# Kernel tuning notes

Hardware: AMD Instinct MI355X
Metric: run time of the kernel (lower is better)

## Reference

```python
import jax, jax.numpy as jnp
import numpy as np

N_HEADS = 16


def apply_rotary_emb(x, cos, sin):
    # x: [B, H, S, hd]; cos/sin: [S, hd//2] (broadcast over B, H)
    xr = x.reshape(x.shape[:-1] + (-1, 2))
    r, i = xr[..., 0], xr[..., 1]
    a = r * cos - i * sin
    b = i * cos + r * sin
    return jnp.stack([a, b], axis=-1).reshape(x.shape).astype(x.dtype)


def setup_inputs() -> dict:
    key = jax.random.key(0)
    ks = jax.random.split(key, 7)
    B, S, D = 2, 2048, 1024
    hd = D // N_HEADS
    x = jax.random.normal(ks[0], (B, S, D), dtype=jnp.float32)
    freqs_cos = jax.random.uniform(ks[1], (S, hd // 2), dtype=jnp.float32)
    freqs_sin = jax.random.uniform(ks[2], (S, hd // 2), dtype=jnp.float32)
    sc = 1.0 / np.sqrt(D)
    Wq = jax.random.normal(ks[3], (D, D), dtype=jnp.float32) * sc
    Wk = jax.random.normal(ks[4], (D, D), dtype=jnp.float32) * sc
    Wv = jax.random.normal(ks[5], (D, D), dtype=jnp.float32) * sc
    Wo = jax.random.normal(ks[6], (D, D), dtype=jnp.float32) * sc
    return {"x": x, "freqs_cos": freqs_cos, "freqs_sin": freqs_sin,
            "Wq": Wq, "Wk": Wk, "Wv": Wv, "Wo": Wo}


def reference(x, freqs_cos, freqs_sin, Wq, Wk, Wv, Wo):
    B, S, D = x.shape
    H = N_HEADS
    hd = D // H
    # QKV projections (nn.Linear: x @ W.T)
    q = (x @ Wq.T).reshape(B, S, H, hd).transpose(0, 2, 1, 3)
    k = (x @ Wk.T).reshape(B, S, H, hd).transpose(0, 2, 1, 3)
    v = (x @ Wv.T).reshape(B, S, H, hd).transpose(0, 2, 1, 3)
    q = apply_rotary_emb(q, freqs_cos, freqs_sin)
    k = apply_rotary_emb(k, freqs_cos, freqs_sin)
    # causal SDPA (scale = 1/sqrt(head_dim), as in F.scaled_dot_product_attention)
    scores = jnp.einsum("bhqd,bhkd->bhqk", q, k) * (1.0 / np.sqrt(hd))
    causal = jnp.tril(jnp.ones((S, S), dtype=bool))
    scores = jnp.where(causal, scores, -jnp.inf)
    probs = jax.nn.softmax(scores, axis=-1)
    attn_out = jnp.einsum("bhqk,bhkd->bhqd", probs, v)
    attn_cat = attn_out.transpose(0, 2, 1, 3).reshape(B, S, D)
    return attn_cat @ Wo.T
```

## Files before the change

### kernel.cpp

```cpp
#include <hip/hip_runtime.h>
#include <hip/hip_bf16.h>
#include <cstdint>

typedef __attribute__((ext_vector_type(8))) short short8;
typedef __attribute__((ext_vector_type(4))) float f32x4;

#define B_  2
#define S_  2048
#define D_  1024
#define H_  16
#define HD  64

static __device__ __forceinline__ float bf2f(unsigned int u16) {
    union { unsigned int i; float f; } v; v.i = u16 << 16; return v.f;
}
static __device__ __forceinline__ unsigned short f2bf(float f) {
    union { float f; unsigned int i; } v; v.f = f;
    unsigned int r = v.i + 0x7FFFu + ((v.i >> 16) & 1u);
    return (unsigned short)(r >> 16);
}
static __device__ __forceinline__ unsigned pack_bf16(float hi, float lo) {
    union { float f; unsigned u; } h, l;
    h.f = hi; l.f = lo;
    return __builtin_amdgcn_perm(h.u + 0x8000u, l.u + 0x8000u, 0x07060302);
}
static __device__ __forceinline__ unsigned cvt_pk_bf16(float a, float b) {
    unsigned r;
    asm("v_cvt_pk_bf16_f32 %0, %1, %2" : "=v"(r) : "v"(a), "v"(b));
    return r;
}
static __device__ __forceinline__ void load_lds_16B(const unsigned short* g, unsigned short* l) {
    __builtin_amdgcn_global_load_lds(
        (const __attribute__((address_space(1))) unsigned int*)g,
        (__attribute__((address_space(3))) unsigned int*)l, 16, 0, 0);
}

__global__ void cvt_all(const float* __restrict__ x,
                        const float* __restrict__ w0, const float* __restrict__ w1,
                        const float* __restrict__ w2, const float* __restrict__ w3,
                        unsigned short* __restrict__ xbf,
                        unsigned short* __restrict__ wdst) {
    int bid = blockIdx.x;
    if (bid < 4096) {
        int i = bid * 256 + threadIdx.x;
        float4 f = ((const float4*)x)[i];
        uint2 o;
        o.x = (unsigned int)f2bf(f.x) | ((unsigned int)f2bf(f.y) << 16);
        o.y = (unsigned int)f2bf(f.z) | ((unsigned int)f2bf(f.w) << 16);
        ((uint2*)xbf)[i] = o;
    } else {
        int wb = bid - 4096;
        int wsel = wb >> 10;
        const float* s = wsel == 0 ? w0 : wsel == 1 ? w1 : wsel == 2 ? w2 : w3;
        int i = (wb & 1023) * 256 + threadIdx.x;
        float4 f = ((const float4*)s)[i];
        uint2 o;
        o.x = (unsigned int)f2bf(f.x) | ((unsigned int)f2bf(f.y) << 16);
        o.y = (unsigned int)f2bf(f.z) | ((unsigned int)f2bf(f.w) << 16);
        ((uint2*)wdst)[(size_t)wsel * 262144 + i] = o;
    }
}

__global__ __launch_bounds__(256) void qkv_gemm(
    const unsigned short* __restrict__ xbf,
    const unsigned short* __restrict__ wq,
    const unsigned short* __restrict__ wk,
    const unsigned short* __restrict__ wv,
    const float* __restrict__ fcos,
    const float* __restrict__ fsin,
    unsigned short* __restrict__ qb,
    unsigned short* __restrict__ kb,
    unsigned short* __restrict__ vb)
{
    __shared__ unsigned short pool[2][2][128 * 32];

    const int tid  = threadIdx.x;
    const int w    = tid >> 6, lane = tid & 63;
    const int l15  = lane & 15, quad = lane >> 4;
    const int wrow = (w >> 1) * 64, wcol = (w & 1) * 64;

    const int m0 = blockIdx.x * 128;
    const int nc = blockIdx.y * 128;
    const int sel = nc >> 10;
    const int n0 = nc & 1023;
    const unsigned short* __restrict__ W = sel == 0 ? wq : (sel == 1 ? wk : wv);

    const int lr = lane >> 2, lc = (lane & 3) * 8;
    const unsigned short* ga = xbf + (size_t)(m0 + w * 16 + lr) * 1024 + lc;
    const unsigned short* gb = W   + (size_t)(n0 + w * 16 + lr) * 1024 + lc;

    f32x4 acc[4][4] = {};

    auto STAGE = [&](int k0, int bufi) {
        load_lds_16B(ga + k0,             &pool[bufi][0][(w * 16) * 32]);
        load_lds_16B(ga + 64 * 1024 + k0, &pool[bufi][0][(64 + w * 16) * 32]);
        load_lds_16B(gb + k0,             &pool[bufi][1][(w * 16) * 32]);
        load_lds_16B(gb + 64 * 1024 + k0, &pool[bufi][1][(64 + w * 16) * 32]);
    };

    STAGE(0, 0);
    __syncthreads();

    int cur = 0;
    for (int k0 = 0; k0 < 1024; k0 += 32) {
        if (k0 + 32 < 1024) STAGE(k0 + 32, cur ^ 1);

        short8 a[4], b[4];
#pragma unroll
        for (int i = 0; i < 4; i++)
            a[i] = *(const short8*)&pool[cur][0][(wrow + i * 16 + l15) * 32 + quad * 8];
#pragma unroll
        for (int j = 0; j < 4; j++)
            b[j] = *(const short8*)&pool[cur][1][(wcol + j * 16 + l15) * 32 + quad * 8];
#pragma unroll
        for (int i = 0; i < 4; i++)
#pragma unroll
            for (int j = 0; j < 4; j++)
                acc[i][j] = __builtin_amdgcn_mfma_f32_16x16x32_bf16(a[i], b[j], acc[i][j], 0, 0, 0);

        __syncthreads();
        cur ^= 1;
    }

    if (sel == 2) {
        unsigned short (*Tt)[136] = reinterpret_cast<unsigned short (*)[136]>(&pool[0][0][0]);
        const int bb  = blockIdx.x >> 4;
        const int m0s = (blockIdx.x & 15) * 128;
        const int h0  = n0 >> 6;
        const int nh  = w & 1;
#pragma unroll
        for (int half = 0; half < 2; half++) {
            __syncthreads();
            if (nh == half) {
#pragma unroll
                for (int i = 0; i < 4; i++)
#pragma unroll
                    for (int j = 0; j < 4; j++) {
                        uint2 pk;
                        pk.x = pack_bf16(acc[i][j][1], acc[i][j][0]);
                        pk.y = pack_bf16(acc[i][j][3], acc[i][j][2]);
                        *(uint2*)&Tt[j * 16 + l15][wrow + i * 16 + quad * 4] = pk;
                    }
            }
            __syncthreads();
            const int row = tid >> 2, cq = tid & 3;
            unsigned short* vrow = vb +
                (((size_t)(bb * H_ + h0 + half)) * HD + row) * S_ + m0s + cq * 32;
#pragma unroll
            for (int k = 0; k < 4; k++) {
                short8 v = *(const short8*)&Tt[row][cq * 32 + k * 8];
                *(short8*)(vrow + k * 8) = v;
            }
        }
    } else {
        unsigned short* __restrict__ Out = sel == 0 ? qb : kb;
        const float qsc = (sel == 0) ? 0.125f * 1.44269504f : 1.0f;
        const int odd = l15 & 1;
#pragma unroll
        for (int i = 0; i < 4; i++)
#pragma unroll
            for (int r = 0; r < 4; r++) {
                int m = m0 + wrow + i * 16 + quad * 4 + r;
                int bb = m >> 11, s = m & 2047;
#pragma unroll
                for (int j = 0; j < 4; j++) {
                    int n = n0 + wcol + j * 16 + l15;
                    int h = n >> 6, d = n & 63;
                    int t = d >> 1;
                    float c  = fcos[s * 32 + t];
                    float si = fsin[s * 32 + t];
                    float own = acc[i][j][r];
                    float oth = __shfl_xor(own, 1, 64);
                    float outv = odd ? (own * c + oth * si) : (own * c - oth * si);
                    Out[(((size_t)(bb * H_ + h) * S_) + s) * HD + d] = f2bf(outv * qsc);
                }
            }
    }
}

__global__ __launch_bounds__(256) void out_gemm(
    const unsigned short* __restrict__ A,
    const unsigned short* __restrict__ Bt,
    float* __restrict__ C)
{
    __shared__ __attribute__((aligned(1024))) unsigned short Apool[2][128 * 64];
    __shared__ __attribute__((aligned(1024))) unsigned short Bpool[2][64 * 64];

    const int tid  = threadIdx.x;
    const int w    = tid >> 6, lane = tid & 63;
    const int l15  = lane & 15, quad = lane >> 4;
    const int wrow = (w >> 1) * 64, wcol = (w & 1) * 32;

    const int m0 = blockIdx.x * 128;
    const int n0 = blockIdx.y * 64;

    const int srow  = lane >> 3;
    const int sslot = (lane & 7) ^ srow;
    const int s7    = l15 & 7;

    f32x4 acc[4][2] = {};

    auto STAGE = [&](int k0, int bufi) {
        const unsigned short* gaa = A + (size_t)m0 * 1024 + k0 + sslot * 8;
        load_lds_16B(gaa + (size_t)(w * 16 + srow) * 1024,          &Apool[bufi][(w * 16) * 64]);
        load_lds_16B(gaa + (size_t)(w * 16 + 8 + srow) * 1024,      &Apool[bufi][(w * 16 + 8) * 64]);
        load_lds_16B(gaa + (size_t)(64 + w * 16 + srow) * 1024,     &Apool[bufi][(64 + w * 16) * 64]);
        load_lds_16B(gaa + (size_t)(64 + w * 16 + 8 + srow) * 1024, &Apool[bufi][(64 + w * 16 + 8) * 64]);
        const unsigned short* gbb = Bt + (size_t)n0 * 1024 + k0 + sslot * 8;
        load_lds_16B(gbb + (size_t)(w * 16 + srow) * 1024,          &Bpool[bufi][(w * 16) * 64]);
        load_lds_16B(gbb + (size_t)(w * 16 + 8 + srow) * 1024,      &Bpool[bufi][(w * 16 + 8) * 64]);
    };

    STAGE(0, 0);
    __syncthreads();

    int cur = 0;
    for (int k0 = 0; k0 < 1024; k0 += 64) {
        if (k0 + 64 < 1024) STAGE(k0 + 64, cur ^ 1);

        short8 a[4][2], b[2][2];
#pragma unroll
        for (int kk = 0; kk < 2; kk++) {
#pragma unroll
            for (int i = 0; i < 4; i++) {
                int row = wrow + i * 16 + l15;
                int slot = (((kk << 2) | quad) ^ s7) << 4;
                a[i][kk] = *(const short8*)((const char*)&Apool[cur][0] + (row << 7) + slot);
            }
#pragma unroll
            for (int j = 0; j < 2; j++) {
                int row = wcol + j * 16 + l15;
                int slot = (((kk << 2) | quad) ^ s7) << 4;
                b[j][kk] = *(const short8*)((const char*)&Bpool[cur][0] + (row << 7) + slot);
            }
        }
#pragma unroll
        for (int kk = 0; kk < 2; kk++)
#pragma unroll
            for (int i = 0; i < 4; i++)
#pragma unroll
                for (int j = 0; j < 2; j++)
                    acc[i][j] = __builtin_amdgcn_mfma_f32_16x16x32_bf16(a[i][kk], b[j][kk], acc[i][j], 0, 0, 0);

        __syncthreads();
        cur ^= 1;
    }

#pragma unroll
    for (int i = 0; i < 4; i++)
#pragma unroll
        for (int r = 0; r < 4; r++) {
            int m = m0 + wrow + i * 16 + quad * 4 + r;
#pragma unroll
            for (int j = 0; j < 2; j++)
                C[(size_t)m * 1024 + n0 + wcol + j * 16 + l15] = acc[i][j][r];
        }
}

__global__ __launch_bounds__(256) void flash_attn_mfma(
    const unsigned short* __restrict__ qb,
    const unsigned short* __restrict__ kb,
    const unsigned short* __restrict__ vT,
    unsigned short* __restrict__ attnc)
{
    __shared__ __attribute__((aligned(1024))) unsigned short Ks[2][2][64][32];
    __shared__ __attribute__((aligned(1024))) unsigned short Vt[64][64];
    __shared__ unsigned short Pls[4][16][72];

    const int bh   = blockIdx.x;
    const int qtb  = blockIdx.y;
    const int jj = qtb & 7, mm = qtb >> 3;
    const int qt = (mm == 0) ? jj : (mm == 1) ? 31 - jj : (mm == 2) ? 8 + jj : 23 - jj;

    const int b    = bh >> 4, h = bh & 15;
    const int tid  = threadIdx.x;
    const int w    = tid >> 6;
    const int lane = tid & 63;
    const int l15  = lane & 15;
    const int quad = lane >> 4;

    const size_t bhS = (size_t)bh * S_;
    const unsigned short* __restrict__ vTb = vT + (size_t)bh * HD * S_;

    short8 qfrag[2];
    {
        const unsigned short* qp = qb + (bhS + qt * 64 + w * 16 + l15) * HD + quad * 8;
        qfrag[0] = *(const short8*)(qp);
        qfrag[1] = *(const short8*)(qp + 32);
    }

    const int ksrow  = lane >> 2;
    const int ksslot = (lane & 3) ^ ((lane >> 3) & 3);
    const int vsrow  = lane >> 3;
    const int vsslot = (lane & 7) ^ vsrow;

    const int ckq = (quad ^ ((l15 >> 1) & 3)) << 4;
    const int s7  = l15 & 7;

    short8 ones;
#pragma unroll
    for (int i = 0; i < 8; i++) ones[i] = (short)0x3F80;

    f32x4 O[4] = {};
    f32x4 Osum = {};
    float mrow = -INFINITY;

    auto STAGE_K = [&](int jt, int bufi) {
        const int j0 = jt * 64;
        const unsigned short* kg = kb + (bhS + j0 + w * 16 + ksrow) * HD + ksslot * 8;
        load_lds_16B(kg,      &Ks[bufi][0][w * 16][0]);
        load_lds_16B(kg + 32, &Ks[bufi][1][w * 16][0]);
    };
    auto STAGE_V = [&](int jt) {
        const int j0 = jt * 64;
        const unsigned short* vg = vTb + (size_t)(w * 16 + vsrow) * S_ + j0 + vsslot * 8;
        load_lds_16B(vg,          &Vt[w * 16][0]);
        load_lds_16B(vg + 8 * S_, &Vt[w * 16 + 8][0]);
    };

    STAGE_K(0, 0);

    for (int jt = 0; jt <= qt; jt++) {
        const int cur = jt & 1;
        asm volatile("s_waitcnt vmcnt(0)" ::: "memory");
        __builtin_amdgcn_s_barrier();

        STAGE_V(jt);
        if (jt < qt) STAGE_K(jt + 1, cur ^ 1);

        const bool diag  = (jt == qt);
        const int  nsub  = diag ? (w + 1) : 4;
        const int  kgmax = (nsub + 1) >> 1;

        f32x4 Sacc[4];
        float tmax = -INFINITY;
        for (int sub = 0; sub < nsub; sub++) {
            f32x4 s = {};
#pragma unroll
            for (int kh = 0; kh < 2; kh++) {
                int bo = ((sub * 16 + l15) << 6) + ckq;
                short8 kf = *(const short8*)((const char*)&Ks[cur][kh][0][0] + bo);
                s = __builtin_amdgcn_mfma_f32_16x16x32_bf16(kf, qfrag[kh], s, 0, 0, 0);
            }
            if (diag) {
#pragma unroll
                for (int r = 0; r < 4; r++)
                    if (sub * 16 + quad * 4 + r > w * 16 + l15) s[r] = -INFINITY;
            }
            float sm = fmaxf(fmaxf(s[0], s[1]), fmaxf(s[2], s[3]));
            tmax = fmaxf(tmax, sm);
            Sacc[sub] = s;
        }
        tmax = fmaxf(tmax, __shfl_xor(tmax, 16, 64));
        tmax = fmaxf(tmax, __shfl_xor(tmax, 32, 64));

        if (__any(tmax > mrow + 8.0f)) {
            float mnew = fmaxf(mrow, tmax);
            float ccr  = __builtin_amdgcn_exp2f(mrow - mnew);
#pragma unroll
            for (int r = 0; r < 4; r++) {
                float ccq = __shfl(ccr, quad * 4 + r, 64);
#pragma unroll
                for (int dt = 0; dt < 4; dt++) O[dt][r] *= ccq;
                Osum[r] *= ccq;
            }
            mrow = mnew;
        }

        for (int sub = 0; sub < nsub; sub++) {
            f32x4 s = Sacc[sub];
            float p0 = __builtin_amdgcn_exp2f(s[0] - mrow);
            float p1 = __builtin_amdgcn_exp2f(s[1] - mrow);
            float p2 = __builtin_amdgcn_exp2f(s[2] - mrow);
            float p3 = __builtin_amdgcn_exp2f(s[3] - mrow);
            uint2 pk;
            pk.x = cvt_pk_bf16(p0, p1);
            pk.y = cvt_pk_bf16(p2, p3);
            *(uint2*)&Pls[w][l15][sub * 16 + quad * 4] = pk;
        }
        if (diag) {
            for (int sub = nsub; sub < 2 * kgmax; sub++) {
                uint2 z; z.x = 0u; z.y = 0u;
                *(uint2*)&Pls[w][l15][sub * 16 + quad * 4] = z;
            }
        }

        if (jt < qt) {
            asm volatile("s_waitcnt vmcnt(2)" ::: "memory");
        } else {
            asm volatile("s_waitcnt vmcnt(0)" ::: "memory");
        }
        __builtin_amdgcn_s_barrier();

        for (int kg = 0; kg < kgmax; kg++) {
            short8 pf = *(const short8*)&Pls[w][l15][kg * 32 + quad * 8];
#pragma unroll
            for (int dt = 0; dt < 4; dt++) {
                int row = dt * 16 + l15;
                int slot = (((kg << 2) | quad) ^ s7) << 4;
                short8 vf = *(const short8*)((const char*)&Vt[0][0] + (row << 7) + slot);
                O[dt] = __builtin_amdgcn_mfma_f32_16x16x32_bf16(pf, vf, O[dt], 0, 0, 0);
            }
            Osum = __builtin_amdgcn_mfma_f32_16x16x32_bf16(pf, ones, Osum, 0, 0, 0);
        }
    }

#pragma unroll
    for (int r = 0; r < 4; r++) {
        float invq = 1.0f / Osum[r];
        int qabs = qt * 64 + w * 16 + quad * 4 + r;
        unsigned short* op = attnc + (((size_t)b * S_ + qabs) * H_ + h) * HD + l15;
#pragma unroll
        for (int dt = 0; dt < 4; dt++)
            op[dt * 16] = f2bf(O[dt][r] * invq);
    }
}

extern "C" void kernel_launch(void* const* d_in, const int* in_sizes, int n_in,
                              void* d_out, int out_size, void* d_ws, size_t ws_size,
                              hipStream_t stream) {
    const float* x    = (const float*)d_in[0];
    const float* fcos = (const float*)d_in[1];
    const float* fsin = (const float*)d_in[2];
    const float* Wq   = (const float*)d_in[3];
    const float* Wk   = (const float*)d_in[4];
    const float* Wv   = (const float*)d_in[5];
    const float* Wo   = (const float*)d_in[6];
    float* out = (float*)d_out;

    unsigned short* ws = (unsigned short*)d_ws;
    unsigned short* xbf = ws;
    unsigned short* wqb = xbf + 4096 * 1024;
    unsigned short* wkb = wqb + 1024 * 1024;
    unsigned short* wvb = wkb + 1024 * 1024;
    unsigned short* wob = wvb + 1024 * 1024;
    unsigned short* qb  = wob + 1024 * 1024;
    unsigned short* kb  = qb + 4096 * 1024;
    unsigned short* vb  = kb + 4096 * 1024;
    unsigned short* attnc = vb + 4096 * 1024;

    cvt_all<<<8192, 256, 0, stream>>>(x, Wq, Wk, Wv, Wo, xbf, wqb);

    qkv_gemm<<<dim3(32, 24), 256, 0, stream>>>(xbf, wqb, wkb, wvb, fcos, fsin, qb, kb, vb);

    flash_attn_mfma<<<dim3(32, 32), 256, 0, stream>>>(qb, kb, vb, attnc);

    out_gemm<<<dim3(32, 16), 256, 0, stream>>>(attnc, wob, out);
}
```

Baseline: 201.7 us.

## Pair causal query tiles per block to share K/V loads and balance work

Each attention block now handles two query tiles, qt and 31-qt, so every block does the same amount of causal work. The K/V tiles staged into LDS are reused by both query tiles, which halves global K/V traffic per query. The grid shrinks from 1024 to 512 blocks. In exchange, register pressure roughly doubles (two sets of O accumulators and Q fragments) and the P scratch buffer doubles, which may reduce occupancy.

```diff
diff --git a/kernel.cpp b/kernel.cpp
--- a/kernel.cpp
+++ b/kernel.cpp
@@ -265,12 +265,12 @@
 {
     __shared__ __attribute__((aligned(1024))) unsigned short Ks[2][2][64][32];
     __shared__ __attribute__((aligned(1024))) unsigned short Vt[64][64];
-    __shared__ unsigned short Pls[4][16][72];
-
-    const int bh   = blockIdx.x;
-    const int qtb  = blockIdx.y;
-    const int jj = qtb & 7, mm = qtb >> 3;
-    const int qt = (mm == 0) ? jj : (mm == 1) ? 31 - jj : (mm == 2) ? 8 + jj : 23 - jj;
+    __shared__ unsigned short Pls[2][4][16][72];
+
+    const int bh    = blockIdx.x;
+    const int qtA   = blockIdx.y;
+    const int qtB   = 31 - qtA;
+    const int jtmax = qtB;
 
     const int b    = bh >> 4, h = bh & 15;
     const int tid  = threadIdx.x;
@@ -282,11 +282,14 @@
     const size_t bhS = (size_t)bh * S_;
     const unsigned short* __restrict__ vTb = vT + (size_t)bh * HD * S_;
 
-    short8 qfrag[2];
+    short8 qfA[2], qfB[2];
     {
-        const unsigned short* qp = qb + (bhS + qt * 64 + w * 16 + l15) * HD + quad * 8;
-        qfrag[0] = *(const short8*)(qp);
-        qfrag[1] = *(const short8*)(qp + 32);
+        const unsigned short* qp = qb + (bhS + qtA * 64 + w * 16 + l15) * HD + quad * 8;
+        qfA[0] = *(const short8*)(qp);
+        qfA[1] = *(const short8*)(qp + 32);
+        const unsigned short* qp2 = qb + (bhS + qtB * 64 + w * 16 + l15) * HD + quad * 8;
+        qfB[0] = *(const short8*)(qp2);
+        qfB[1] = *(const short8*)(qp2 + 32);
     }
 
     const int ksrow  = lane >> 2;
@@ -301,9 +304,11 @@
 #pragma unroll
     for (int i = 0; i < 8; i++) ones[i] = (short)0x3F80;
 
-    f32x4 O[4] = {};
-    f32x4 Osum = {};
-    float mrow = -INFINITY;
+    f32x4 OA[4] = {}, OB[4] = {};
+    f32x4 OsA = {}, OsB = {};
+    float mA = -INFINITY, mB = -INFINITY;
+
+    int cur = 0;
 
     auto STAGE_K = [&](int jt, int bufi) {
         const int j0 = jt * 64;
@@ -318,20 +323,10 @@
         load_lds_16B(vg + 8 * S_, &Vt[w * 16 + 8][0]);
     };
 
-    STAGE_K(0, 0);
-
-    for (int jt = 0; jt <= qt; jt++) {
-        const int cur = jt & 1;
-        asm volatile("s_waitcnt vmcnt(0)" ::: "memory");
-        __builtin_amdgcn_s_barrier();
-
-        STAGE_V(jt);
-        if (jt < qt) STAGE_K(jt + 1, cur ^ 1);
-
-        const bool diag  = (jt == qt);
-        const int  nsub  = diag ? (w + 1) : 4;
-        const int  kgmax = (nsub + 1) >> 1;
-
+    auto QKSM = [&](const short8* qf, float& mrow, f32x4* O, f32x4& Osum,
+                    int psel, bool diag) -> int {
+        const int nsub  = diag ? (w + 1) : 4;
+        const int kgmax = (nsub + 1) >> 1;
         f32x4 Sacc[4];
         float tmax = -INFINITY;
         for (int sub = 0; sub < nsub; sub++) {
@@ -340,7 +335,7 @@
             for (int kh = 0; kh < 2; kh++) {
                 int bo = ((sub * 16 + l15) << 6) + ckq;
                 short8 kf = *(const short8*)((const char*)&Ks[cur][kh][0][0] + bo);
-                s = __builtin_amdgcn_mfma_f32_16x16x32_bf16(kf, qfrag[kh], s, 0, 0, 0);
+                s = __builtin_amdgcn_mfma_f32_16x16x32_bf16(kf, qf[kh], s, 0, 0, 0);
             }
             if (diag) {
 #pragma unroll
@@ -376,24 +371,20 @@
             uint2 pk;
             pk.x = cvt_pk_bf16(p0, p1);
             pk.y = cvt_pk_bf16(p2, p3);
-            *(uint2*)&Pls[w][l15][sub * 16 + quad * 4] = pk;
+            *(uint2*)&Pls[psel][w][l15][sub * 16 + quad * 4] = pk;
         }
         if (diag) {
             for (int sub = nsub; sub < 2 * kgmax; sub++) {
                 uint2 z; z.x = 0u; z.y = 0u;
-                *(uint2*)&Pls[w][l15][sub * 16 + quad * 4] = z;
-            }
-        }
-
-        if (jt < qt) {
-            asm volatile("s_waitcnt vmcnt(2)" ::: "memory");
-        } else {
-            asm volatile("s_waitcnt vmcnt(0)" ::: "memory");
-        }
-        __builtin_amdgcn_s_barrier();
-
+                *(uint2*)&Pls[psel][w][l15][sub * 16 + quad * 4] = z;
+            }
+        }
+        return kgmax;
+    };
+
+    auto PV = [&](int psel, int kgmax, f32x4* O, f32x4& Osum) {
         for (int kg = 0; kg < kgmax; kg++) {
-            short8 pf = *(const short8*)&Pls[w][l15][kg * 32 + quad * 8];
+            short8 pf = *(const short8*)&Pls[psel][w][l15][kg * 32 + quad * 8];
 #pragma unroll
             for (int dt = 0; dt < 4; dt++) {
                 int row = dt * 16 + l15;
@@ -403,16 +394,52 @@
             }
             Osum = __builtin_amdgcn_mfma_f32_16x16x32_bf16(pf, ones, Osum, 0, 0, 0);
         }
+    };
+
+    STAGE_K(0, 0);
+
+    for (int jt = 0; jt <= jtmax; jt++) {
+        cur = jt & 1;
+        asm volatile("s_waitcnt vmcnt(0)" ::: "memory");
+        __builtin_amdgcn_s_barrier();
+
+        STAGE_V(jt);
+        if (jt < jtmax) STAGE_K(jt + 1, cur ^ 1);
+
+        const bool doA = (jt <= qtA);
+        int kgA = 0;
+        if (doA) kgA = QKSM(qfA, mA, OA, OsA, 0, jt == qtA);
+        int kgB = QKSM(qfB, mB, OB, OsB, 1, jt == jtmax);
+
+        if (jt < jtmax) {
+            asm volatile("s_waitcnt vmcnt(2)" ::: "memory");
+        } else {
+            asm volatile("s_waitcnt vmcnt(0)" ::: "memory");
+        }
+        __builtin_amdgcn_s_barrier();
+
+        if (doA) PV(0, kgA, OA, OsA);
+        PV(1, kgB, OB, OsB);
     }
 
 #pragma unroll
     for (int r = 0; r < 4; r++) {
-        float invq = 1.0f / Osum[r];
-        int qabs = qt * 64 + w * 16 + quad * 4 + r;
-        unsigned short* op = attnc + (((size_t)b * S_ + qabs) * H_ + h) * HD + l15;
-#pragma unroll
-        for (int dt = 0; dt < 4; dt++)
-            op[dt * 16] = f2bf(O[dt][r] * invq);
+        {
+            float invq = 1.0f / OsA[r];
+            int qabs = qtA * 64 + w * 16 + quad * 4 + r;
+            unsigned short* op = attnc + (((size_t)b * S_ + qabs) * H_ + h) * HD + l15;
+#pragma unroll
+            for (int dt = 0; dt < 4; dt++)
+                op[dt * 16] = f2bf(OA[dt][r] * invq);
+        }
+        {
+            float invq = 1.0f / OsB[r];
+            int qabs = qtB * 64 + w * 16 + quad * 4 + r;
+            unsigned short* op = attnc + (((size_t)b * S_ + qabs) * H_ + h) * HD + l15;
+#pragma unroll
+            for (int dt = 0; dt < 4; dt++)
+                op[dt * 16] = f2bf(OB[dt][r] * invq);
+        }
     }
 }
 
@@ -443,7 +470,7 @@
 
     qkv_gemm<<<dim3(32, 24), 256, 0, stream>>>(xbf, wqb, wkb, wvb, fcos, fsin, qb, kb, vb);
 
-    flash_attn_mfma<<<dim3(32, 32), 256, 0, stream>>>(qb, kb, vb, attnc);
+    flash_attn_mfma<<<dim3(32, 16), 256, 0, stream>>>(qb, kb, vb, attnc);
 
     out_gemm<<<dim3(32, 16), 256, 0, stream>>>(attnc, wob, out);
 }
```

After: 204.1 us. About the same (+1.2%).
